# Performance work log

Measured on AMD Instinct MI355X. Metric: run time of the kernel, lower is better.

Reference implementation:

```python
import jax, jax.numpy as jnp
import numpy as np


def setup_inputs() -> dict:
    key = jax.random.key(0)
    k1, k2 = jax.random.split(key)
    B, C, T = 32, 384, 1024
    x = jax.random.normal(k1, (B, C, T), dtype=jnp.float32)
    duration = jax.random.randint(k2, (B, T), 0, 8, dtype=jnp.int32)
    return {"x": x, "duration": duration, "max_len": 7168}


def reference(x, duration, max_len):
    # x: [B, C, T], duration: [B, T] int32
    # Vectorized equivalent of per-phoneme repeat_interleave + pad.
    csum = jnp.cumsum(duration, axis=1)              # [B, T] exclusive-right boundaries
    mel_len = csum[:, -1]                            # [B] total expanded length
    frames = jnp.arange(max_len, dtype=jnp.int32)    # [L]
    # phoneme index owning each output frame: searchsorted skips zero-duration phonemes
    idx = jax.vmap(lambda c: jnp.searchsorted(c, frames, side='right'))(csum)  # [B, L]
    idx = jnp.clip(idx, 0, x.shape[2] - 1)
    out = jnp.take_along_axis(x, idx[:, None, :], axis=2)  # [B, C, L] gather along T
    valid = frames[None, :] < mel_len[:, None]              # [B, L] padding mask
    out = jnp.where(valid[:, None, :], out, jnp.zeros((), dtype=x.dtype))
    return out, mel_len.astype(jnp.int32)
```

## Files before the change

### kernel.cpp

```cpp
#include <hip/hip_runtime.h>


#define B_ 32
#define C_ 384
#define T_ 1024
#define MAXLEN_ 7168
#define FT_ 7
#define CPB_ 8
#define NT_ 256
#define NWG_ (B_ * (C_ / CPB_) * FT_)
#define NXCD_ 8

typedef float f32x4 __attribute__((ext_vector_type(4)));

__global__ __launch_bounds__(NT_) void lr_fused_kernel(
    const int* __restrict__ dur,
    const float* __restrict__ x,
    float* __restrict__ out,
    float* __restrict__ mel_out)
{
    const int tid = threadIdx.x;

    const int bid  = blockIdx.x;
    const int wgid = (bid & (NXCD_ - 1)) * (NWG_ / NXCD_) + (bid >> 3);
    const int ftile = wgid % FT_;
    const int rest  = wgid / FT_;
    const int cblk  = rest % (C_ / CPB_);
    const int b     = rest / (C_ / CPB_);
    const int f0    = ftile << 10;

    __shared__ int s_tok[1024];
    __shared__ int s_w[NT_ / 64];

    const int4 d4 = ((const int4*)(dur + b * T_))[tid];
    const int sum4 = d4.x + d4.y + d4.z + d4.w;

    const int lane = tid & 63;
    const int wave = tid >> 6;
    int sc = sum4;
    #pragma unroll
    for (int d = 1; d < 64; d <<= 1) {
        int n = __shfl_up(sc, d, 64);
        if (lane >= d) sc += n;
    }
    if (lane == 63) s_w[wave] = sc;
    __syncthreads();

    int woff = 0;
    #pragma unroll
    for (int w = 0; w < NT_ / 64; ++w)
        woff += (w < wave) ? s_w[w] : 0;
    const int mel = s_w[0] + s_w[1] + s_w[2] + s_w[3];

    if (ftile == 0 && cblk == 0 && tid == 0)
        mel_out[b] = (float)mel;

    float* ob = out + ((size_t)b * C_ + cblk * CPB_) * MAXLEN_ + f0 + (tid << 2);

    if (f0 >= mel) {
        const f32x4 z = {0.0f, 0.0f, 0.0f, 0.0f};
        #pragma unroll
        for (int cc = 0; cc < CPB_; ++cc)
            __builtin_nontemporal_store(z, (f32x4*)(ob + (size_t)cc * MAXLEN_));
        return;
    }

    ((int4*)s_tok)[tid] = make_int4(-1, -1, -1, -1);
    __syncthreads();

    const int st = woff + sc - sum4;

    {
        const int base_tok = tid << 2;
        const int s0 = st;
        const int s1 = s0 + d4.x;
        const int s2 = s1 + d4.y;
        const int s3 = s2 + d4.z;
        const int starts[4] = { s0, s1, s2, s3 };
        const int lens[4]   = { d4.x, d4.y, d4.z, d4.w };
        #pragma unroll
        for (int k = 0; k < 4; ++k) {
            int lo = starts[k] - f0;
            int hi = lo + lens[k];
            lo = lo < 0 ? 0 : lo;
            hi = hi > 1024 ? 1024 : hi;
            for (int p = lo; p < hi; ++p)
                s_tok[p] = base_tok + k;
        }
    }
    __syncthreads();

    const int4 t4 = ((const int4*)s_tok)[tid];

    const float* xb = x + ((size_t)b * C_ + cblk * CPB_) * T_;

    #pragma unroll
    for (int cc = 0; cc < CPB_; ++cc) {
        const float* __restrict__ xr = xb + cc * T_;
        f32x4 v;
        v.x = (t4.x >= 0) ? xr[t4.x] : 0.0f;
        v.y = (t4.y >= 0) ? xr[t4.y] : 0.0f;
        v.z = (t4.z >= 0) ? xr[t4.z] : 0.0f;
        v.w = (t4.w >= 0) ? xr[t4.w] : 0.0f;
        __builtin_nontemporal_store(v, (f32x4*)(ob + (size_t)cc * MAXLEN_));
    }
}

extern "C" void kernel_launch(void* const* d_in, const int* in_sizes, int n_in,
                              void* d_out, int out_size, void* d_ws, size_t ws_size,
                              hipStream_t stream) {
    const float* x   = (const float*)d_in[0];
    const int*   dur = (const int*)d_in[1];

    float* out = (float*)d_out;
    float* mel_out = out + (size_t)B_ * C_ * MAXLEN_;

    lr_fused_kernel<<<NWG_, NT_, 0, stream>>>(dur, x, out, mel_out);
}
```

Before: 72.61 us.

## Process all frame tiles per workgroup, computing duration scan once

Each workgroup now covers one (batch, channel-block) pair and loops over the seven 1024-frame tiles itself, instead of launching one workgroup per tile. The duration prefix scan is computed once per workgroup rather than repeated for every tile, and a double-buffered token map in shared memory lets consecutive tiles proceed with fewer hazards. The cost is a 7x smaller grid (1536 workgroups), so there is less parallelism to hide memory latency, and the tiles within a workgroup are handled one after another.

```diff
diff --git a/kernel.cpp b/kernel.cpp
--- a/kernel.cpp
+++ b/kernel.cpp
@@ -8,7 +8,8 @@
 #define FT_ 7
 #define CPB_ 8
 #define NT_ 256
-#define NWG_ (B_ * (C_ / CPB_) * FT_)
+#define NCG_ (C_ / CPB_)
+#define NWG_ (B_ * NCG_)
 #define NXCD_ 8
 
 typedef float f32x4 __attribute__((ext_vector_type(4)));
@@ -23,13 +24,10 @@
 
     const int bid  = blockIdx.x;
     const int wgid = (bid & (NXCD_ - 1)) * (NWG_ / NXCD_) + (bid >> 3);
-    const int ftile = wgid % FT_;
-    const int rest  = wgid / FT_;
-    const int cblk  = rest % (C_ / CPB_);
-    const int b     = rest / (C_ / CPB_);
-    const int f0    = ftile << 10;
+    const int cblk = wgid % NCG_;
+    const int b    = wgid / NCG_;
 
-    __shared__ int s_tok[1024];
+    __shared__ int s_tok[2][1024];
     __shared__ int s_w[NT_ / 64];
 
     const int4 d4 = ((const int4*)(dur + b * T_))[tid];
@@ -52,57 +50,65 @@
         woff += (w < wave) ? s_w[w] : 0;
     const int mel = s_w[0] + s_w[1] + s_w[2] + s_w[3];
 
-    if (ftile == 0 && cblk == 0 && tid == 0)
+    if (cblk == 0 && tid == 0)
         mel_out[b] = (float)mel;
 
-    float* ob = out + ((size_t)b * C_ + cblk * CPB_) * MAXLEN_ + f0 + (tid << 2);
+    const int st = woff + sc - sum4;
+    const int s0 = st;
+    const int s1 = s0 + d4.x;
+    const int s2 = s1 + d4.y;
+    const int s3 = s2 + d4.z;
+    const int send = s3 + d4.w;
 
-    if (f0 >= mel) {
-        const f32x4 z = {0.0f, 0.0f, 0.0f, 0.0f};
+    const int nvt = (mel + 1023) >> 10;
+
+    const float* xb  = x   + ((size_t)b * C_ + cblk * CPB_) * T_;
+    float*       ob0 = out + ((size_t)b * C_ + cblk * CPB_) * MAXLEN_ + (tid << 2);
+
+    for (int ft = 0; ft < nvt; ++ft) {
+        int* buf = s_tok[ft & 1];
+        const int f0 = ft << 10;
+
+        ((int4*)buf)[tid] = make_int4(-1, -1, -1, -1);
+        __syncthreads();
+
+        if (st < f0 + 1024 && send > f0) {
+            const int base_tok = tid << 2;
+            const int starts[4] = { s0, s1, s2, s3 };
+            const int lens[4]   = { d4.x, d4.y, d4.z, d4.w };
+            #pragma unroll
+            for (int k = 0; k < 4; ++k) {
+                int lo = starts[k] - f0;
+                int hi = lo + lens[k];
+                lo = lo < 0 ? 0 : lo;
+                hi = hi > 1024 ? 1024 : hi;
+                for (int p = lo; p < hi; ++p)
+                    buf[p] = base_tok + k;
+            }
+        }
+        __syncthreads();
+
+        const int4 t4 = ((const int4*)buf)[tid];
+        float* ob = ob0 + f0;
+
+        #pragma unroll
+        for (int cc = 0; cc < CPB_; ++cc) {
+            const float* __restrict__ xr = xb + cc * T_;
+            f32x4 v;
+            v.x = (t4.x >= 0) ? xr[t4.x] : 0.0f;
+            v.y = (t4.y >= 0) ? xr[t4.y] : 0.0f;
+            v.z = (t4.z >= 0) ? xr[t4.z] : 0.0f;
+            v.w = (t4.w >= 0) ? xr[t4.w] : 0.0f;
+            __builtin_nontemporal_store(v, (f32x4*)(ob + (size_t)cc * MAXLEN_));
+        }
+    }
+
+    const f32x4 z = {0.0f, 0.0f, 0.0f, 0.0f};
+    for (int ft = nvt; ft < FT_; ++ft) {
+        float* ob = ob0 + (ft << 10);
         #pragma unroll
         for (int cc = 0; cc < CPB_; ++cc)
             __builtin_nontemporal_store(z, (f32x4*)(ob + (size_t)cc * MAXLEN_));
-        return;
-    }
-
-    ((int4*)s_tok)[tid] = make_int4(-1, -1, -1, -1);
-    __syncthreads();
-
-    const int st = woff + sc - sum4;
-
-    {
-        const int base_tok = tid << 2;
-        const int s0 = st;
-        const int s1 = s0 + d4.x;
-        const int s2 = s1 + d4.y;
-        const int s3 = s2 + d4.z;
-        const int starts[4] = { s0, s1, s2, s3 };
-        const int lens[4]   = { d4.x, d4.y, d4.z, d4.w };
-        #pragma unroll
-        for (int k = 0; k < 4; ++k) {
-            int lo = starts[k] - f0;
-            int hi = lo + lens[k];
-            lo = lo < 0 ? 0 : lo;
-            hi = hi > 1024 ? 1024 : hi;
-            for (int p = lo; p < hi; ++p)
-                s_tok[p] = base_tok + k;
-        }
-    }
-    __syncthreads();
-
-    const int4 t4 = ((const int4*)s_tok)[tid];
-
-    const float* xb = x + ((size_t)b * C_ + cblk * CPB_) * T_;
-
-    #pragma unroll
-    for (int cc = 0; cc < CPB_; ++cc) {
-        const float* __restrict__ xr = xb + cc * T_;
-        f32x4 v;
-        v.x = (t4.x >= 0) ? xr[t4.x] : 0.0f;
-        v.y = (t4.y >= 0) ? xr[t4.y] : 0.0f;
-        v.z = (t4.z >= 0) ? xr[t4.z] : 0.0f;
-        v.w = (t4.w >= 0) ? xr[t4.w] : 0.0f;
-        __builtin_nontemporal_store(v, (f32x4*)(ob + (size_t)cc * MAXLEN_));
     }
 }
 
```

Result: slower. 74.64 us (+2.8%).

## Stage x rows in LDS and gather from shared memory with 16-bit token map

Applied to the files above, without the earlier changes.

Each workgroup now loads its x rows fully and coalesced into LDS, then does the per-frame gather from LDS instead of scattered global loads. The token map shrinks to 16-bit entries, and its init is merged into the first barrier, removing one sync. Channels per block drop from 8 to 4, doubling workgroup count to fit the LDS buffer. The cost is loading whole x rows even for frames that do not use them, plus 16KB of LDS per block.

```diff
diff --git a/kernel.cpp b/kernel.cpp
--- a/kernel.cpp
+++ b/kernel.cpp
@@ -6,9 +6,10 @@
 #define T_ 1024
 #define MAXLEN_ 7168
 #define FT_ 7
-#define CPB_ 8
+#define CPB_ 4
 #define NT_ 256
-#define NWG_ (B_ * (C_ / CPB_) * FT_)
+#define NCG_ (C_ / CPB_)
+#define NWG_ (FT_ * NCG_ * B_)
 #define NXCD_ 8
 
 typedef float f32x4 __attribute__((ext_vector_type(4)));
@@ -25,11 +26,12 @@
     const int wgid = (bid & (NXCD_ - 1)) * (NWG_ / NXCD_) + (bid >> 3);
     const int ftile = wgid % FT_;
     const int rest  = wgid / FT_;
-    const int cblk  = rest % (C_ / CPB_);
-    const int b     = rest / (C_ / CPB_);
+    const int cblk  = rest % NCG_;
+    const int b     = rest / NCG_;
     const int f0    = ftile << 10;
 
-    __shared__ int s_tok[1024];
+    __shared__ float s_x[CPB_][T_];
+    __shared__ unsigned short s_map[1024];
     __shared__ int s_w[NT_ / 64];
 
     const int4 d4 = ((const int4*)(dur + b * T_))[tid];
@@ -44,6 +46,8 @@
         if (lane >= d) sc += n;
     }
     if (lane == 63) s_w[wave] = sc;
+
+    ((int2*)s_map)[tid] = make_int2(-1, -1);
     __syncthreads();
 
     int woff = 0;
@@ -65,12 +69,13 @@
         return;
     }
 
-    ((int4*)s_tok)[tid] = make_int4(-1, -1, -1, -1);
-    __syncthreads();
-
-    const int st = woff + sc - sum4;
+    const float* xb = x + ((size_t)b * C_ + cblk * CPB_) * T_;
+    #pragma unroll
+    for (int r = 0; r < CPB_; ++r)
+        ((f32x4*)s_x[r])[tid] = ((const f32x4*)(xb + r * T_))[tid];
 
     {
+        const int st = woff + sc - sum4;
         const int base_tok = tid << 2;
         const int s0 = st;
         const int s1 = s0 + d4.x;
@@ -85,23 +90,26 @@
             lo = lo < 0 ? 0 : lo;
             hi = hi > 1024 ? 1024 : hi;
             for (int p = lo; p < hi; ++p)
-                s_tok[p] = base_tok + k;
+                s_map[p] = (unsigned short)(base_tok + k);
         }
     }
     __syncthreads();
 
-    const int4 t4 = ((const int4*)s_tok)[tid];
-
-    const float* xb = x + ((size_t)b * C_ + cblk * CPB_) * T_;
+    const uint2 m = ((const uint2*)s_map)[tid];
+    const unsigned int t0 = m.x & 0xFFFFu, t1 = m.x >> 16;
+    const unsigned int t2 = m.y & 0xFFFFu, t3 = m.y >> 16;
 
     #pragma unroll
     for (int cc = 0; cc < CPB_; ++cc) {
-        const float* __restrict__ xr = xb + cc * T_;
+        const float a0 = s_x[cc][t0 & 1023u];
+        const float a1 = s_x[cc][t1 & 1023u];
+        const float a2 = s_x[cc][t2 & 1023u];
+        const float a3 = s_x[cc][t3 & 1023u];
         f32x4 v;
-        v.x = (t4.x >= 0) ? xr[t4.x] : 0.0f;
-        v.y = (t4.y >= 0) ? xr[t4.y] : 0.0f;
-        v.z = (t4.z >= 0) ? xr[t4.z] : 0.0f;
-        v.w = (t4.w >= 0) ? xr[t4.w] : 0.0f;
+        v.x = (t0 <= 1023u) ? a0 : 0.0f;
+        v.y = (t1 <= 1023u) ? a1 : 0.0f;
+        v.z = (t2 <= 1023u) ? a2 : 0.0f;
+        v.w = (t3 <= 1023u) ? a3 : 0.0f;
         __builtin_nontemporal_store(v, (f32x4*)(ob + (size_t)cc * MAXLEN_));
     }
 }
```

New measurement: 67.38 us. 7.2% less time.
